# Performance work log

Hardware: AMD Instinct MI355X
Metric: run time of the kernel (lower is better)

Reference implementation:

```python
import jax, jax.numpy as jnp
import numpy as np

B, S, HID = 2, 2048, 2048
H, KV, D = 16, 4, 128
EPS = 1e-6


def rms_norm(x, w, eps=EPS):
    # Qwen3.5 convention: (1 + weight) * RMSNorm(x), weight init 0
    v = jnp.mean(x * x, axis=-1, keepdims=True)
    return (1.0 + w) * (x * jax.lax.rsqrt(v + eps))


def rotate_half(x):
    x1, x2 = jnp.split(x, 2, axis=-1)
    return jnp.concatenate([-x2, x1], axis=-1)


def apply_rope(x, cos, sin):
    # x: [B,S,h,D]; cos/sin: [S,D]
    c = cos[None, :, None, :]
    s = sin[None, :, None, :]
    return x * c + rotate_half(x) * s


def setup_inputs():
    key = jax.random.key(0)
    ks = jax.random.split(key, 8)
    sc = 0.02
    hidden_states = jax.random.normal(ks[0], (B, S, HID), jnp.float32)
    past_key_value = jnp.zeros((B, 2, KV, S, D), jnp.float32)
    pos = jnp.arange(S, dtype=jnp.float32)
    inv_freq = 1.0 / (10000.0 ** (jnp.arange(0, D, 2, dtype=jnp.float32) / D))
    ang = pos[:, None] * inv_freq[None, :]                    # [S, D/2]
    cos = jnp.concatenate([jnp.cos(ang), jnp.cos(ang)], -1)   # [S, D]
    sin = jnp.concatenate([jnp.sin(ang), jnp.sin(ang)], -1)
    rope_rotary_cos_sin = jnp.stack([cos, sin], axis=1)       # [S, 2, D]
    context_lengths = jnp.full((B,), S, dtype=jnp.int32)
    kvcache_start_index = jnp.zeros((B,), dtype=jnp.int32)
    Wq = jax.random.normal(ks[1], (HID, H * D * 2), jnp.float32) * sc
    Wk = jax.random.normal(ks[2], (HID, KV * D), jnp.float32) * sc
    Wv = jax.random.normal(ks[3], (HID, KV * D), jnp.float32) * sc
    Wo = jax.random.normal(ks[4], (H * D, HID), jnp.float32) * sc
    q_norm_w = jax.random.normal(ks[5], (D,), jnp.float32) * sc
    k_norm_w = jax.random.normal(ks[6], (D,), jnp.float32) * sc
    return {"hidden_states": hidden_states, "past_key_value": past_key_value,
            "rope_rotary_cos_sin": rope_rotary_cos_sin,
            "context_lengths": context_lengths,
            "kvcache_start_index": kvcache_start_index,
            "Wq": Wq, "Wk": Wk, "Wv": Wv, "Wo": Wo,
            "q_norm_w": q_norm_w, "k_norm_w": k_norm_w}


def reference(hidden_states, past_key_value, rope_rotary_cos_sin,
              context_lengths, kvcache_start_index,
              Wq, Wk, Wv, Wo, q_norm_w, k_norm_w):
    # projections
    q_out = jnp.einsum('bsc,cd->bsd', hidden_states, Wq).reshape(B, S, H, 2 * D)
    query, gate = jnp.split(q_out, 2, axis=-1)                # each [B,S,H,D]
    k = jnp.einsum('bsc,cd->bsd', hidden_states, Wk).reshape(B, S, KV, D)
    v = jnp.einsum('bsc,cd->bsd', hidden_states, Wv).reshape(B, S, KV, D)
    # per-head QK RMSNorm
    query = rms_norm(query, q_norm_w)
    k = rms_norm(k, k_norm_w)
    # RoPE
    cos, sin = rope_rotary_cos_sin[:, 0, :], rope_rotary_cos_sin[:, 1, :]
    query = apply_rope(query, cos, sin)
    k = apply_rope(k, cos, sin)
    # write KV cache (prefill at start index 0)
    present = past_key_value.at[:, 0, :, :S, :].set(jnp.transpose(k, (0, 2, 1, 3)))
    present = present.at[:, 1, :, :S, :].set(jnp.transpose(v, (0, 2, 1, 3)))
    # GQA causal attention
    group = H // KV
    k_r = jnp.repeat(k, group, axis=2)                        # [B,S,H,D]
    v_r = jnp.repeat(v, group, axis=2)
    scores = jnp.einsum('bqhd,bkhd->bhqk', query, k_r) / jnp.sqrt(jnp.float32(D))
    causal = jnp.tril(jnp.ones((S, S), dtype=bool))
    scores = jnp.where(causal[None, None], scores, jnp.float32(-1e30))
    probs = jax.nn.softmax(scores, axis=-1)
    attn = jnp.einsum('bhqk,bkhd->bqhd', probs, v_r)          # [B,S,H,D]
    # sigmoid gating + output proj
    attn = attn * jax.nn.sigmoid(gate)
    out = jnp.einsum('bsd,dc->bsc', attn.reshape(B, S, H * D), Wo)
    return out, present
```

## Files before the change

### kernel.cpp

```cpp
#include <hip/hip_runtime.h>
#include <hip/hip_bf16.h>
#include <cstdint>
#include <cstddef>

#define BB   2
#define SS   2048
#define HIDD 2048
#define HH   16
#define KVH  4
#define DD   128
#define NQKV 5120
#define MM   4096

typedef unsigned short u16t;
typedef __attribute__((ext_vector_type(8))) short s16x8;
typedef __attribute__((ext_vector_type(4))) short s16x4;
typedef __attribute__((ext_vector_type(4))) float f32x4;

__device__ __forceinline__ u16t f2bf(float f) {
  unsigned u = __float_as_uint(f);
  u += 0x7fffu + ((u >> 16) & 1u);
  return (u16t)(u >> 16);
}
__device__ __forceinline__ float bf2f(u16t h) {
  return __uint_as_float(((unsigned)h) << 16);
}
__device__ __forceinline__ void gload_lds16(const void* g, void* l) {
  __builtin_amdgcn_global_load_lds(
      (const __attribute__((address_space(1))) unsigned int*)g,
      (__attribute__((address_space(3))) unsigned int*)l, 16, 0, 0);
}
__device__ __forceinline__ unsigned cvtpk_bf16(float lo, float hi) {
  unsigned r;
  asm("v_cvt_pk_bf16_f32 %0, %1, %2" : "=v"(r) : "v"(lo), "v"(hi));
  return r;
}
__device__ __forceinline__ f32x4 fmax4(f32x4 a, f32x4 b) {
  f32x4 r;
  r[0] = fmaxf(a[0], b[0]); r[1] = fmaxf(a[1], b[1]);
  r[2] = fmaxf(a[2], b[2]); r[3] = fmaxf(a[3], b[3]);
  return r;
}
template <int N>
__device__ __forceinline__ void waitvm() {
  static_assert(N == 0 || N == 3 || N == 4 || N == 6 || N == 8, "add literal");
  if constexpr (N == 0)      asm volatile("s_waitcnt vmcnt(0)" ::: "memory");
  else if constexpr (N == 3) asm volatile("s_waitcnt vmcnt(3)" ::: "memory");
  else if constexpr (N == 4) asm volatile("s_waitcnt vmcnt(4)" ::: "memory");
  else if constexpr (N == 6) asm volatile("s_waitcnt vmcnt(6)" ::: "memory");
  else if constexpr (N == 8) asm volatile("s_waitcnt vmcnt(8)" ::: "memory");
}

__global__ __launch_bounds__(256) void prep_all(const float* __restrict__ hidden,
                                                const float* __restrict__ Wq,
                                                const float* __restrict__ Wk,
                                                const float* __restrict__ Wv,
                                                const float* __restrict__ Wo,
                                                u16t* __restrict__ Xb,
                                                u16t* __restrict__ Wt,
                                                u16t* __restrict__ Wot) {
  __shared__ float lds[64 * 65];
  int bid = blockIdx.x;
  int t = threadIdx.x;
  if (bid < 4096) {
    size_t i = ((size_t)bid * 256 + t) * 8;
    f32x4 v0 = *(const f32x4*)(hidden + i);
    f32x4 v1 = *(const f32x4*)(hidden + i + 4);
    s16x8 o;
    o[0] = (short)f2bf(v0[0]); o[1] = (short)f2bf(v0[1]);
    o[2] = (short)f2bf(v0[2]); o[3] = (short)f2bf(v0[3]);
    o[4] = (short)f2bf(v1[0]); o[5] = (short)f2bf(v1[1]);
    o[6] = (short)f2bf(v1[2]); o[7] = (short)f2bf(v1[3]);
    *(s16x8*)(Xb + i) = o;
    return;
  }
  bid -= 4096;
  const float* src; u16t* dst; int N;
  if (bid < 2048)      { src = Wq; dst = Wt;                         N = 4096; }
  else if (bid < 2304) { src = Wk; dst = Wt + (size_t)4096 * HIDD;   N = 512;  bid -= 2048; }
  else if (bid < 2560) { src = Wv; dst = Wt + (size_t)4608 * HIDD;   N = 512;  bid -= 2304; }
  else                 { src = Wo; dst = Wot;                        N = 2048; bid -= 2560; }
  const int ktiles = HIDD / 64;
  int n0 = (bid / ktiles) << 6;
  int k0 = (bid % ktiles) << 6;
#pragma unroll
  for (int i = 0; i < 16; i++) {
    int idx = i * 256 + t;
    int r = idx >> 6, c = idx & 63;
    lds[c * 65 + r] = src[(size_t)(k0 + r) * N + n0 + c];
  }
  __syncthreads();
#pragma unroll
  for (int i = 0; i < 2; i++) {
    int idx = i * 256 + t;
    int rr = idx >> 3, k8 = (idx & 7) * 8;
    s16x8 o;
#pragma unroll
    for (int e = 0; e < 8; e++) o[e] = (short)f2bf(lds[rr * 65 + k8 + e]);
    *(s16x8*)(dst + (size_t)(n0 + rr) * HIDD + k0 + k8) = o;
  }
}

__device__ __forceinline__ s16x8 ldsfrag(const char* half, int r, int g) {
  return *(const s16x8*)(half + r * 64 + ((g ^ ((r >> 1) & 3)) << 4));
}
template <int NL>
__device__ __forceinline__ void stage_half(char* ldsbase, const u16t* gbase,
                                           int K, int kcol, int tid) {
#pragma unroll
  for (int i = 0; i < NL; i++) {
    int o16 = i * 512 + tid;
    int r = o16 >> 2;
    int cs = (o16 & 3) ^ ((r >> 1) & 3);
    gload_lds16(gbase + (size_t)r * K + kcol + cs * 8, ldsbase + o16 * 16);
  }
}

template <int BN, typename CT>
__global__ __launch_bounds__(512, 2) void gemm8(const u16t* __restrict__ A,
                                                const u16t* __restrict__ Bt,
                                                CT* __restrict__ C,
                                                int M, int N, int K) {
  constexpr int NLB = BN / 128;
  constexpr int AHALF = 16384, ASLOT = 32768;
  constexpr int BHALF = BN * 64, BSLOT = 2 * BHALF;
  constexpr int PAIR = 2 + NLB;
  constexpr int NI = BN / 64;
  extern __shared__ __align__(16) char lds[];
  char* As = lds;
  char* Bs = lds + 2 * ASLOT;
  int tid = threadIdx.x, lane = tid & 63, w = tid >> 6;
  int wm = w >> 2, wn = w & 3;
  int cpx = gridDim.x >> 3;
  int wgid = (blockIdx.x & 7) * cpx + (blockIdx.x >> 3);
  int bm = wgid & 15, bn = wgid >> 4;
  int m0 = bm << 8, n0 = bn * BN;
  const u16t* Ag = A + (size_t)m0 * K;
  const u16t* Bg = Bt + (size_t)n0 * K;
  const int NT = K >> 6;

  stage_half<2>(As, Ag, K, 0, tid);
  stage_half<NLB>(Bs, Bg, K, 0, tid);
  stage_half<2>(As + AHALF, Ag, K, 32, tid);
  stage_half<NLB>(Bs + BHALF, Bg, K, 32, tid);
  stage_half<2>(As + ASLOT, Ag, K, 64, tid);
  stage_half<NLB>(Bs + BSLOT, Bg, K, 64, tid);
  waitvm<2 * PAIR>();
  __builtin_amdgcn_s_barrier();

  const f32x4 fz = {0.f, 0.f, 0.f, 0.f};
  f32x4 acc[8][NI];
#pragma unroll
  for (int i = 0; i < 8; i++)
#pragma unroll
    for (int j = 0; j < NI; j++) acc[i][j] = fz;
  s16x8 afr[4], bfr[NI];
  int g = lane >> 4;
  int rA = (lane & 15) + wm * 128;
  int rB = (lane & 15) + wn * (BN / 4);

  for (int kt = 0; kt < NT; kt++) {
    int cur = kt & 1;
    char* Acur = As + cur * ASLOT;
    char* Bcur = Bs + cur * BSLOT;
    char* Anxt = As + (cur ^ 1) * ASLOT;
    char* Bnxt = Bs + (cur ^ 1) * BSLOT;
#pragma unroll
    for (int ni = 0; ni < NI; ni++) bfr[ni] = ldsfrag(Bcur, rB + ni * 16, g);
#pragma unroll
    for (int mi = 0; mi < 4; mi++) afr[mi] = ldsfrag(Acur, rA + mi * 16, g);
    if (kt + 1 < NT) stage_half<2>(Anxt + AHALF, Ag, K, (kt + 1) * 64 + 32, tid);
    __builtin_amdgcn_s_barrier();
    asm volatile("s_waitcnt lgkmcnt(0)" ::: "memory");
    __builtin_amdgcn_s_setprio(1);
#pragma unroll
    for (int mi = 0; mi < 4; mi++)
#pragma unroll
      for (int ni = 0; ni < NI; ni++)
        acc[mi][ni] = __builtin_amdgcn_mfma_f32_16x16x32_bf16(afr[mi], bfr[ni], acc[mi][ni], 0, 0, 0);
    __builtin_amdgcn_s_setprio(0);
    __builtin_amdgcn_s_barrier();
#pragma unroll
    for (int mi = 0; mi < 4; mi++) afr[mi] = ldsfrag(Acur, rA + 64 + mi * 16, g);
    if (kt + 1 < NT) stage_half<NLB>(Bnxt + BHALF, Bg, K, (kt + 1) * 64 + 32, tid);
    __builtin_amdgcn_s_barrier();
    asm volatile("s_waitcnt lgkmcnt(0)" ::: "memory");
    __builtin_amdgcn_s_setprio(1);
#pragma unroll
    for (int mi = 0; mi < 4; mi++)
#pragma unroll
      for (int ni = 0; ni < NI; ni++)
        acc[4 + mi][ni] = __builtin_amdgcn_mfma_f32_16x16x32_bf16(afr[mi], bfr[ni], acc[4 + mi][ni], 0, 0, 0);
    __builtin_amdgcn_s_setprio(0);
    if (kt + 1 < NT) waitvm<2 * PAIR>();
    else             waitvm<0>();
    __builtin_amdgcn_s_barrier();
#pragma unroll
    for (int ni = 0; ni < NI; ni++) bfr[ni] = ldsfrag(Bcur + BHALF, rB + ni * 16, g);
#pragma unroll
    for (int mi = 0; mi < 4; mi++) afr[mi] = ldsfrag(Acur + AHALF, rA + mi * 16, g);
    if (kt + 2 < NT) stage_half<2>(Acur, Ag, K, (kt + 2) * 64, tid);
    __builtin_amdgcn_s_barrier();
    asm volatile("s_waitcnt lgkmcnt(0)" ::: "memory");
    __builtin_amdgcn_s_setprio(1);
#pragma unroll
    for (int mi = 0; mi < 4; mi++)
#pragma unroll
      for (int ni = 0; ni < NI; ni++)
        acc[mi][ni] = __builtin_amdgcn_mfma_f32_16x16x32_bf16(afr[mi], bfr[ni], acc[mi][ni], 0, 0, 0);
    __builtin_amdgcn_s_setprio(0);
    __builtin_amdgcn_s_barrier();
#pragma unroll
    for (int mi = 0; mi < 4; mi++) afr[mi] = ldsfrag(Acur + AHALF, rA + 64 + mi * 16, g);
    if (kt + 2 < NT) stage_half<NLB>(Bcur, Bg, K, (kt + 2) * 64, tid);
    __builtin_amdgcn_s_barrier();
    asm volatile("s_waitcnt lgkmcnt(0)" ::: "memory");
    __builtin_amdgcn_s_setprio(1);
#pragma unroll
    for (int mi = 0; mi < 4; mi++)
#pragma unroll
      for (int ni = 0; ni < NI; ni++)
        acc[4 + mi][ni] = __builtin_amdgcn_mfma_f32_16x16x32_bf16(afr[mi], bfr[ni], acc[4 + mi][ni], 0, 0, 0);
    __builtin_amdgcn_s_setprio(0);
    if (kt < NT - 1) {
      if (kt + 2 < NT) waitvm<2 * PAIR>();
      else             waitvm<PAIR>();
    }
    __builtin_amdgcn_s_barrier();
  }
#pragma unroll
  for (int mi = 0; mi < 8; mi++)
#pragma unroll
    for (int ni = 0; ni < NI; ni++) {
      int row0 = m0 + wm * 128 + mi * 16 + ((lane >> 4) << 2);
      int col = n0 + wn * (BN / 4) + ni * 16 + (lane & 15);
#pragma unroll
      for (int j = 0; j < 4; j++) {
        if constexpr (sizeof(CT) == 2)
          C[(size_t)(row0 + j) * N + col] = f2bf(acc[mi][ni][j]);
        else
          C[(size_t)(row0 + j) * N + col] = acc[mi][ni][j];
      }
    }
}

__global__ __launch_bounds__(256) void gemm_kv(const u16t* __restrict__ A,
                                               const u16t* __restrict__ Bt,
                                               u16t* __restrict__ Cqkv,
                                               float* __restrict__ present,
                                               u16t* __restrict__ Vtb,
                                               int K) {
  __shared__ __align__(16) char As[128 * 64];
  __shared__ __align__(16) char Bs[128 * 64];
  int tid = threadIdx.x;
  int lane = tid & 63;
  int w = tid >> 6;
  int cpx = gridDim.x >> 3;
  int wgid = ((int)blockIdx.x & 7) * cpx + ((int)blockIdx.x >> 3);
  const int mtiles = MM >> 7;
  int bm = wgid % mtiles;
  int bn = wgid / mtiles;
  int m0 = bm << 7, n0 = bn << 7;
  int wr = (w >> 1) * 64, wc = (w & 1) * 64;

  const f32x4 fz = {0.f, 0.f, 0.f, 0.f};
  f32x4 acc[4][4];
#pragma unroll
  for (int i = 0; i < 4; i++)
#pragma unroll
    for (int j = 0; j < 4; j++) acc[i][j] = fz;

  for (int k0 = 0; k0 < K; k0 += 32) {
    __syncthreads();
#pragma unroll
    for (int i = 0; i < 2; i++) {
      int idx = i * 256 + tid;
      int r = idx >> 2, c = idx & 3;
      int csrc = c ^ ((r >> 1) & 3);
      gload_lds16(A + (size_t)(m0 + r) * K + k0 + csrc * 8, As + idx * 16);
      gload_lds16(Bt + (size_t)(n0 + r) * K + k0 + csrc * 8, Bs + idx * 16);
    }
    __syncthreads();
    s16x8 af[4], bf[4];
    int g = lane >> 4;
#pragma unroll
    for (int mi = 0; mi < 4; mi++) {
      int r = wr + mi * 16 + (lane & 15);
      af[mi] = *(const s16x8*)(As + r * 64 + ((g ^ ((r >> 1) & 3)) << 4));
    }
#pragma unroll
    for (int ni = 0; ni < 4; ni++) {
      int r = wc + ni * 16 + (lane & 15);
      bf[ni] = *(const s16x8*)(Bs + r * 64 + ((g ^ ((r >> 1) & 3)) << 4));
    }
#pragma unroll
    for (int mi = 0; mi < 4; mi++)
#pragma unroll
      for (int ni = 0; ni < 4; ni++)
        acc[mi][ni] = __builtin_amdgcn_mfma_f32_16x16x32_bf16(af[mi], bf[ni], acc[mi][ni], 0, 0, 0);
  }
  if (bn < 4) {
#pragma unroll
    for (int mi = 0; mi < 4; mi++)
#pragma unroll
      for (int ni = 0; ni < 4; ni++) {
        int row0 = m0 + wr + mi * 16 + ((lane >> 4) << 2);
        int col = n0 + wc + ni * 16 + (lane & 15);
#pragma unroll
        for (int j = 0; j < 4; j++)
          Cqkv[(size_t)(row0 + j) * NQKV + 4096 + col] = f2bf(acc[mi][ni][j]);
      }
  } else {
#pragma unroll
    for (int mi = 0; mi < 4; mi++)
#pragma unroll
      for (int ni = 0; ni < 4; ni++) {
        int row0 = m0 + wr + mi * 16 + ((lane >> 4) << 2);
        int vcol = (n0 - 512) + wc + ni * 16 + (lane & 15);
        int kv = vcol >> 7, d = vcol & 127;
        int bb = row0 >> 11, sp = row0 & 2047;
        size_t pbase = (((size_t)(bb * 2 * KVH + KVH + kv)) * SS + sp) * DD + d;
#pragma unroll
        for (int j = 0; j < 4; j++)
          present[pbase + (size_t)j * DD] = acc[mi][ni][j];
        s16x4 pk;
        pk[0] = (short)f2bf(acc[mi][ni][0]);
        pk[1] = (short)f2bf(acc[mi][ni][1]);
        pk[2] = (short)f2bf(acc[mi][ni][2]);
        pk[3] = (short)f2bf(acc[mi][ni][3]);
        *(s16x4*)(Vtb + ((size_t)(bb * KVH + kv) * DD + d) * SS + sp) = pk;
      }
  }
}

__global__ __launch_bounds__(256) void qk_norm_rope(const u16t* __restrict__ Cqkv,
                                                    const float* __restrict__ rope,
                                                    const float* __restrict__ qw,
                                                    const float* __restrict__ kw,
                                                    u16t* __restrict__ Qb,
                                                    u16t* __restrict__ Kb,
                                                    u16t* __restrict__ Gs,
                                                    float* __restrict__ present) {
  int wid = blockIdx.x * 4 + (threadIdx.x >> 6);
  int lane = threadIdx.x & 63;
  const int NQ = BB * SS * HH;
  if (wid < NQ) {
    int b = wid >> 15;
    int rem = wid & 32767;
    int s = rem >> 4, h = rem & 15;
    const u16t* base = Cqkv + (size_t)(b * SS + s) * NQKV + h * 256;
    float xlo = bf2f(base[lane]), xhi = bf2f(base[64 + lane]);
    float ss = xlo * xlo + xhi * xhi;
    ss += __shfl_xor(ss, 1);  ss += __shfl_xor(ss, 2);  ss += __shfl_xor(ss, 4);
    ss += __shfl_xor(ss, 8);  ss += __shfl_xor(ss, 16); ss += __shfl_xor(ss, 32);
    float r = rsqrtf(ss * (1.f / 128.f) + 1e-6f);
    float qlo = xlo * r * (1.f + qw[lane]);
    float qhi = xhi * r * (1.f + qw[64 + lane]);
    const float* cs = rope + (size_t)s * 256;
    float clo = cs[lane], chi = cs[64 + lane];
    float slo = cs[128 + lane], shi = cs[192 + lane];
    const float SC = 0.08838834764831845f * 1.4426950408889634f;
    float olo = (qlo * clo - qhi * slo) * SC;
    float ohi = (qhi * chi + qlo * shi) * SC;
    size_t qoff = (((size_t)b * HH + h) * SS + s) * DD;
    Qb[qoff + lane] = f2bf(olo);
    Qb[qoff + 64 + lane] = f2bf(ohi);
    float glo = bf2f(base[128 + lane]), ghi = bf2f(base[192 + lane]);
    size_t goff = ((size_t)(b * SS + s)) * (HH * DD) + h * DD;
    Gs[goff + lane] = f2bf(1.f / (1.f + __expf(-glo)));
    Gs[goff + 64 + lane] = f2bf(1.f / (1.f + __expf(-ghi)));
  } else {
    int wid2 = wid - NQ;
    int b = wid2 >> 13;
    int rem = wid2 & 8191;
    int s = rem >> 2, kv = rem & 3;
    const u16t* base = Cqkv + (size_t)(b * SS + s) * NQKV + 4096 + kv * 128;
    float xlo = bf2f(base[lane]), xhi = bf2f(base[64 + lane]);
    float ss = xlo * xlo + xhi * xhi;
    ss += __shfl_xor(ss, 1);  ss += __shfl_xor(ss, 2);  ss += __shfl_xor(ss, 4);
    ss += __shfl_xor(ss, 8);  ss += __shfl_xor(ss, 16); ss += __shfl_xor(ss, 32);
    float r = rsqrtf(ss * (1.f / 128.f) + 1e-6f);
    float klo = xlo * r * (1.f + kw[lane]);
    float khi = xhi * r * (1.f + kw[64 + lane]);
    const float* cs = rope + (size_t)s * 256;
    float clo = cs[lane], chi = cs[64 + lane];
    float slo = cs[128 + lane], shi = cs[192 + lane];
    float olo = klo * clo - khi * slo;
    float ohi = khi * chi + klo * shi;
    size_t koff = (((size_t)b * KVH + kv) * SS + s) * DD;
    Kb[koff + lane] = f2bf(olo);
    Kb[koff + 64 + lane] = f2bf(ohi);
    size_t poff = (((size_t)(b * 2 * KVH + kv)) * SS + s) * DD;
    present[poff + lane] = olo;
    present[poff + 64 + lane] = ohi;
  }
}

__global__ __launch_bounds__(256, 2) void attn_kernel(const u16t* __restrict__ Qb,
                                                      const u16t* __restrict__ Kb,
                                                      const u16t* __restrict__ Vtb,
                                                      const u16t* __restrict__ Gs,
                                                      u16t* __restrict__ AttG) {
  __shared__ __align__(16) char Ks[2 * 16384];
  __shared__ __align__(16) char Vs[2 * 16384];
  __shared__ __align__(16) char Ps[4 * 2048];

  int tid = threadIdx.x, lane = tid & 63, w = tid >> 6;
  int x = blockIdx.x & 7;
  int b = x >> 2, kv = x & 3;
  int rr = blockIdx.x >> 3;
  int h = kv * 4 + (rr & 3);
  int p = rr >> 2;

  const u16t* Kbase = Kb + (((size_t)(b * KVH + kv)) * SS) * DD;
  const u16t* Vbase = Vtb + (((size_t)(b * KVH + kv)) * DD) * SS;

  auto stageK = [&](int kt, int buf) {
#pragma unroll
    for (int i = 0; i < 4; i++) {
      int idx = i * 256 + tid;
      int r_ = idx >> 4, c_ = idx & 15;
      gload_lds16(Kbase + (size_t)(kt * 64 + r_) * DD + (c_ ^ (r_ & 7)) * 8,
                  Ks + buf * 16384 + idx * 16);
    }
  };
  auto stageV = [&](int kt, int buf) {
#pragma unroll
    for (int i = 0; i < 4; i++) {
      int idx = i * 256 + tid;
      int r_ = idx >> 3, c_ = idx & 7;
      gload_lds16(Vbase + (size_t)r_ * SS + kt * 64 + (c_ ^ (r_ & 7)) * 8,
                  Vs + buf * 16384 + idx * 16);
    }
  };

  const f32x4 fz = {0.f, 0.f, 0.f, 0.f};
  int g = lane >> 4;
  int q15 = lane & 15;
  int q7 = q15 & 7;
  char* pq = Ps + w * 2048 + q15 * 128;
  int cur = 0;

  int ka[4][4];
#pragma unroll
  for (int ni = 0; ni < 4; ni++)
#pragma unroll
    for (int ks = 0; ks < 4; ks++)
      ka[ni][ks] = (ni * 16 + q15) * 256 + (((ks * 4 + g) ^ q7) << 4);
  int va[2][8];
#pragma unroll
  for (int ks2 = 0; ks2 < 2; ks2++)
#pragma unroll
    for (int f = 0; f < 8; f++)
      va[ks2][f] = (f * 16 + q15) * 128 + (((ks2 * 4 + g) ^ q7) << 4);
  int pr_[2];
#pragma unroll
  for (int ks2 = 0; ks2 < 2; ks2++) pr_[ks2] = ((ks2 * 4 + g) ^ q7) << 4;
  int pw_[4];
#pragma unroll
  for (int ni = 0; ni < 4; ni++)
    pw_[ni] = (((ni * 2 + (g >> 1)) ^ q7) << 4) + ((g & 1) << 3);

  stageK(0, 0);
  stageV(0, 0);

  for (int seg = 0; seg < 2; seg++) {
    int qt = (seg == 0) ? (31 - p) : p;
    const u16t* Qbase = Qb + (((size_t)(b * HH + h)) * SS + qt * 64) * DD;
    s16x8 qf[4];
    {
      const u16t* qrow = Qbase + (size_t)(w * 16 + q15) * DD + g * 8;
#pragma unroll
      for (int ks = 0; ks < 4; ks++) qf[ks] = *(const s16x8*)(qrow + ks * 32);
    }
    f32x4 acco[8];
#pragma unroll
    for (int f = 0; f < 8; f++) acco[f] = fz;
    float mrun = -INFINITY, lrun = 0.f;

    if (seg == 0) {
      asm volatile("s_waitcnt vmcnt(0)" ::: "memory");
      __builtin_amdgcn_s_barrier();
    }

    for (int kt = 0; kt <= qt; kt++) {
      bool havenext = (kt < qt) || (seg == 0);
      if (havenext) {
        int nk = (kt < qt) ? (kt + 1) : 0;
        stageK(nk, cur ^ 1);
        stageV(nk, cur ^ 1);
      }
      const char* kc = Ks + (cur << 14);
      const char* vc = Vs + (cur << 14);
      f32x4 accs[4];
#pragma unroll
      for (int ni = 0; ni < 4; ni++) accs[ni] = fz;
#pragma unroll
      for (int ni = 0; ni < 4; ni++)
#pragma unroll
        for (int ks = 0; ks < 4; ks++) {
          s16x8 bfk = *(const s16x8*)(kc + ka[ni][ks]);
          accs[ni] = __builtin_amdgcn_mfma_f32_16x16x32_bf16(bfk, qf[ks], accs[ni], 0, 0, 0);
        }
      if (kt == qt) {
        int ql = w * 16 + q15;
#pragma unroll
        for (int ni = 0; ni < 4; ni++)
#pragma unroll
          for (int j = 0; j < 4; j++) {
            int kl = ni * 16 + (g << 2) + j;
            if (kl > ql) accs[ni][j] = -1e30f;
          }
      }
      f32x4 m4 = fmax4(fmax4(accs[0], accs[1]), fmax4(accs[2], accs[3]));
      float mt = fmaxf(fmaxf(m4[0], m4[1]), fmaxf(m4[2], m4[3]));
      mt = fmaxf(mt, __shfl_xor(mt, 16));
      mt = fmaxf(mt, __shfl_xor(mt, 32));
      float mnew = fmaxf(mrun, mt);
      float alpha = __builtin_amdgcn_exp2f(mrun - mnew);
      mrun = mnew;
#pragma unroll
      for (int ni = 0; ni < 4; ni++)
#pragma unroll
        for (int j = 0; j < 4; j++)
          accs[ni][j] = __builtin_amdgcn_exp2f(accs[ni][j] - mnew);
      f32x4 s4 = (accs[0] + accs[1]) + (accs[2] + accs[3]);
      float rs = (s4[0] + s4[1]) + (s4[2] + s4[3]);
      rs += __shfl_xor(rs, 16);
      rs += __shfl_xor(rs, 32);
      lrun = lrun * alpha + rs;
      float ar[4];
#pragma unroll
      for (int j = 0; j < 4; j++) ar[j] = __shfl(alpha, (g << 2) + j);
#pragma unroll
      for (int f = 0; f < 8; f++)
#pragma unroll
        for (int j = 0; j < 4; j++) acco[f][j] *= ar[j];

#pragma unroll
      for (int ni = 0; ni < 4; ni++) {
        uint2 pk;
        pk.x = cvtpk_bf16(accs[ni][0], accs[ni][1]);
        pk.y = cvtpk_bf16(accs[ni][2], accs[ni][3]);
        *(uint2*)(pq + pw_[ni]) = pk;
      }
#pragma unroll
      for (int ks2 = 0; ks2 < 2; ks2++) {
        s16x8 pa = *(const s16x8*)(pq + pr_[ks2]);
#pragma unroll
        for (int f = 0; f < 8; f++) {
          s16x8 vf = *(const s16x8*)(vc + va[ks2][f]);
          acco[f] = __builtin_amdgcn_mfma_f32_16x16x32_bf16(pa, vf, acco[f], 0, 0, 0);
        }
      }
      if (havenext) {
        asm volatile("s_waitcnt vmcnt(0)" ::: "memory");
        __builtin_amdgcn_s_barrier();
        cur ^= 1;
      }
    }
    float lr[4];
#pragma unroll
    for (int j = 0; j < 4; j++) lr[j] = __shfl(lrun, (g << 2) + j);
#pragma unroll
    for (int f = 0; f < 8; f++) {
      int d = f * 16 + q15;
#pragma unroll
      for (int j = 0; j < 4; j++) {
        int srow = qt * 64 + w * 16 + (g << 2) + j;
        float o = acco[f][j] / lr[j];
        size_t off = ((size_t)b * SS + srow) * (HH * DD) + h * DD + d;
        float gt = bf2f(Gs[off]);
        AttG[off] = f2bf(o * gt);
      }
    }
  }
}

extern "C" void kernel_launch(void* const* d_in, const int* in_sizes, int n_in,
                              void* d_out, int out_size, void* d_ws, size_t ws_size,
                              hipStream_t stream) {
  const float* hidden = (const float*)d_in[0];
  const float* rope   = (const float*)d_in[2];
  const float* Wq     = (const float*)d_in[5];
  const float* Wk     = (const float*)d_in[6];
  const float* Wv     = (const float*)d_in[7];
  const float* Wo     = (const float*)d_in[8];
  const float* qw     = (const float*)d_in[9];
  const float* kw     = (const float*)d_in[10];
  float* out = (float*)d_out;
  float* present = out + (size_t)BB * SS * HIDD;

  char* ws = (char*)d_ws;
  u16t* Xb    = (u16t*)(ws);
  u16t* Wt    = (u16t*)(ws + 16777216);
  u16t* Wot   = (u16t*)(ws + 37748736);
  u16t* Cqkv  = (u16t*)(ws + 46137344);
  u16t* Qb    = (u16t*)(ws + 88080384);
  u16t* Kb    = (u16t*)(ws + 104857600);
  u16t* Vtb   = (u16t*)(ws + 109051904);
  u16t* Gs    = (u16t*)(ws + 113246208);
  u16t* AttG  = Xb;

  (void)hipFuncSetAttribute(reinterpret_cast<const void*>(gemm8<256, u16t>),
                            hipFuncAttributeMaxDynamicSharedMemorySize, 131072);
  (void)hipFuncSetAttribute(reinterpret_cast<const void*>(gemm8<128, float>),
                            hipFuncAttributeMaxDynamicSharedMemorySize, 98304);

  prep_all<<<4096 + 3584, 256, 0, stream>>>(hidden, Wq, Wk, Wv, Wo, Xb, Wt, Wot);
  gemm8<256, u16t><<<(MM / 256) * (4096 / 256), 512, 131072, stream>>>(Xb, Wt, Cqkv, MM, NQKV, HIDD);
  gemm_kv<<<(MM / 128) * (1024 / 128), 256, 0, stream>>>(
      Xb, Wt + (size_t)4096 * HIDD, Cqkv, present, Vtb, HIDD);
  qk_norm_rope<<<(BB * SS * (HH + KVH)) / 4, 256, 0, stream>>>(Cqkv, rope, qw, kw, Qb, Kb, Gs, present);
  attn_kernel<<<BB * HH * (SS / 128), 256, 0, stream>>>(Qb, Kb, Vtb, Gs, AttG);
  gemm8<128, float><<<(MM / 256) * (HIDD / 128), 512, 98304, stream>>>(AttG, Wot, out, MM, HIDD, HIDD);
}
```

Baseline: 265.5 us.

## Fuse Q RMSNorm, RoPE and gate sigmoid into the Q projection GEMM epilogue

Adds a gemm8q kernel in which each 256-column tile covers one head's 128 query columns plus its 128 gate columns. The query half is staged through swizzled LDS so each row can be RMS-normalized, rotated with RoPE and written straight to Qb. The gate half gets its sigmoid applied and goes straight to Gs. This removes the bf16 round trip of Q and the gate through Cqkv and shrinks the separate norm kernel to K heads only. In exchange the GEMM epilogue gets longer, runs per-row serial loops and does extra LDS traffic.

```diff
diff --git a/kernel.cpp b/kernel.cpp
--- a/kernel.cpp
+++ b/kernel.cpp
@@ -244,6 +244,179 @@
     }
 }
 
+__global__ __launch_bounds__(512, 2) void gemm8q(const u16t* __restrict__ A,
+                                                 const u16t* __restrict__ Bt,
+                                                 const float* __restrict__ rope,
+                                                 const float* __restrict__ qw,
+                                                 u16t* __restrict__ Qb,
+                                                 u16t* __restrict__ Gs,
+                                                 int K) {
+  constexpr int NLB = 2, AHALF = 16384, ASLOT = 32768;
+  constexpr int BHALF = 16384, BSLOT = 32768;
+  constexpr int PAIR = 4, NI = 4;
+  extern __shared__ __align__(16) char lds[];
+  char* As = lds;
+  char* Bs = lds + 2 * ASLOT;
+  int tid = threadIdx.x, lane = tid & 63, w = tid >> 6;
+  int wm = w >> 2, wn = w & 3;
+  int cpx = gridDim.x >> 3;
+  int wgid = (blockIdx.x & 7) * cpx + (blockIdx.x >> 3);
+  int bm = wgid & 15, bn = wgid >> 4;
+  int m0 = bm << 8, n0 = bn << 8;
+  const u16t* Ag = A + (size_t)m0 * K;
+  const u16t* Bg = Bt + (size_t)n0 * K;
+  const int NT = K >> 6;
+
+  stage_half<2>(As, Ag, K, 0, tid);
+  stage_half<NLB>(Bs, Bg, K, 0, tid);
+  stage_half<2>(As + AHALF, Ag, K, 32, tid);
+  stage_half<NLB>(Bs + BHALF, Bg, K, 32, tid);
+  stage_half<2>(As + ASLOT, Ag, K, 64, tid);
+  stage_half<NLB>(Bs + BSLOT, Bg, K, 64, tid);
+  waitvm<2 * PAIR>();
+  __builtin_amdgcn_s_barrier();
+
+  const f32x4 fz = {0.f, 0.f, 0.f, 0.f};
+  f32x4 acc[8][NI];
+#pragma unroll
+  for (int i = 0; i < 8; i++)
+#pragma unroll
+    for (int j = 0; j < NI; j++) acc[i][j] = fz;
+  s16x8 afr[4], bfr[NI];
+  int g = lane >> 4;
+  int rA = (lane & 15) + wm * 128;
+  int rB = (lane & 15) + wn * 64;
+
+  for (int kt = 0; kt < NT; kt++) {
+    int cur = kt & 1;
+    char* Acur = As + cur * ASLOT;
+    char* Bcur = Bs + cur * BSLOT;
+    char* Anxt = As + (cur ^ 1) * ASLOT;
+    char* Bnxt = Bs + (cur ^ 1) * BSLOT;
+#pragma unroll
+    for (int ni = 0; ni < NI; ni++) bfr[ni] = ldsfrag(Bcur, rB + ni * 16, g);
+#pragma unroll
+    for (int mi = 0; mi < 4; mi++) afr[mi] = ldsfrag(Acur, rA + mi * 16, g);
+    if (kt + 1 < NT) stage_half<2>(Anxt + AHALF, Ag, K, (kt + 1) * 64 + 32, tid);
+    __builtin_amdgcn_s_barrier();
+    asm volatile("s_waitcnt lgkmcnt(0)" ::: "memory");
+    __builtin_amdgcn_s_setprio(1);
+#pragma unroll
+    for (int mi = 0; mi < 4; mi++)
+#pragma unroll
+      for (int ni = 0; ni < NI; ni++)
+        acc[mi][ni] = __builtin_amdgcn_mfma_f32_16x16x32_bf16(afr[mi], bfr[ni], acc[mi][ni], 0, 0, 0);
+    __builtin_amdgcn_s_setprio(0);
+    __builtin_amdgcn_s_barrier();
+#pragma unroll
+    for (int mi = 0; mi < 4; mi++) afr[mi] = ldsfrag(Acur, rA + 64 + mi * 16, g);
+    if (kt + 1 < NT) stage_half<NLB>(Bnxt + BHALF, Bg, K, (kt + 1) * 64 + 32, tid);
+    __builtin_amdgcn_s_barrier();
+    asm volatile("s_waitcnt lgkmcnt(0)" ::: "memory");
+    __builtin_amdgcn_s_setprio(1);
+#pragma unroll
+    for (int mi = 0; mi < 4; mi++)
+#pragma unroll
+      for (int ni = 0; ni < NI; ni++)
+        acc[4 + mi][ni] = __builtin_amdgcn_mfma_f32_16x16x32_bf16(afr[mi], bfr[ni], acc[4 + mi][ni], 0, 0, 0);
+    __builtin_amdgcn_s_setprio(0);
+    if (kt + 1 < NT) waitvm<2 * PAIR>();
+    else             waitvm<0>();
+    __builtin_amdgcn_s_barrier();
+#pragma unroll
+    for (int ni = 0; ni < NI; ni++) bfr[ni] = ldsfrag(Bcur + BHALF, rB + ni * 16, g);
+#pragma unroll
+    for (int mi = 0; mi < 4; mi++) afr[mi] = ldsfrag(Acur + AHALF, rA + mi * 16, g);
+    if (kt + 2 < NT) stage_half<2>(Acur, Ag, K, (kt + 2) * 64, tid);
+    __builtin_amdgcn_s_barrier();
+    asm volatile("s_waitcnt lgkmcnt(0)" ::: "memory");
+    __builtin_amdgcn_s_setprio(1);
+#pragma unroll
+    for (int mi = 0; mi < 4; mi++)
+#pragma unroll
+      for (int ni = 0; ni < NI; ni++)
+        acc[mi][ni] = __builtin_amdgcn_mfma_f32_16x16x32_bf16(afr[mi], bfr[ni], acc[mi][ni], 0, 0, 0);
+    __builtin_amdgcn_s_setprio(0);
+    __builtin_amdgcn_s_barrier();
+#pragma unroll
+    for (int mi = 0; mi < 4; mi++) afr[mi] = ldsfrag(Acur + AHALF, rA + 64 + mi * 16, g);
+    if (kt + 2 < NT) stage_half<NLB>(Bcur, Bg, K, (kt + 2) * 64, tid);
+    __builtin_amdgcn_s_barrier();
+    asm volatile("s_waitcnt lgkmcnt(0)" ::: "memory");
+    __builtin_amdgcn_s_setprio(1);
+#pragma unroll
+    for (int mi = 0; mi < 4; mi++)
+#pragma unroll
+      for (int ni = 0; ni < NI; ni++)
+        acc[4 + mi][ni] = __builtin_amdgcn_mfma_f32_16x16x32_bf16(afr[mi], bfr[ni], acc[4 + mi][ni], 0, 0, 0);
+    __builtin_amdgcn_s_setprio(0);
+    if (kt < NT - 1) {
+      if (kt + 2 < NT) waitvm<2 * PAIR>();
+      else             waitvm<PAIR>();
+    }
+    __builtin_amdgcn_s_barrier();
+  }
+
+  int h = bn;
+  float* qbuf = (float*)lds;
+  if (wn < 2) {
+#pragma unroll
+    for (int mi = 0; mi < 8; mi++)
+#pragma unroll
+      for (int ni = 0; ni < NI; ni++) {
+        int rl0 = wm * 128 + mi * 16 + ((lane >> 4) << 2);
+        int c = wn * 64 + ni * 16 + (lane & 15);
+        int gr = c >> 4;
+#pragma unroll
+        for (int j = 0; j < 4; j++) {
+          int rl = rl0 + j;
+          qbuf[rl * 128 + (((gr ^ ((rl >> 2) & 7)) << 4) | (c & 15))] = acc[mi][ni][j];
+        }
+      }
+  } else {
+#pragma unroll
+    for (int mi = 0; mi < 8; mi++)
+#pragma unroll
+      for (int ni = 0; ni < NI; ni++) {
+        int row0 = m0 + wm * 128 + mi * 16 + ((lane >> 4) << 2);
+        int d = (wn - 2) * 64 + ni * 16 + (lane & 15);
+#pragma unroll
+        for (int j = 0; j < 4; j++) {
+          int bb = (row0 + j) >> 11, s = (row0 + j) & 2047;
+          float gv = acc[mi][ni][j];
+          Gs[((size_t)(bb * SS + s)) * (HH * DD) + h * DD + d] =
+              f2bf(1.f / (1.f + __expf(-gv)));
+        }
+      }
+  }
+  __syncthreads();
+  float qwl = qw[lane], qwh = qw[64 + lane];
+  const float SC = 0.08838834764831845f * 1.4426950408889634f;
+  for (int r2 = 0; r2 < 32; r2++) {
+    int rl = w * 32 + r2;
+    int row0 = m0 + rl;
+    int bb = row0 >> 11, s = row0 & 2047;
+    int swz = ((rl >> 2) & 7) << 4;
+    int cl = lane, ch = 64 + lane;
+    float xlo = qbuf[rl * 128 + ((((cl >> 4) << 4) ^ swz) | (cl & 15))];
+    float xhi = qbuf[rl * 128 + ((((ch >> 4) << 4) ^ swz) | (ch & 15))];
+    float ss2 = xlo * xlo + xhi * xhi;
+    ss2 += __shfl_xor(ss2, 1);  ss2 += __shfl_xor(ss2, 2);  ss2 += __shfl_xor(ss2, 4);
+    ss2 += __shfl_xor(ss2, 8);  ss2 += __shfl_xor(ss2, 16); ss2 += __shfl_xor(ss2, 32);
+    float r = rsqrtf(ss2 * (1.f / 128.f) + 1e-6f);
+    float qlo = xlo * r * (1.f + qwl);
+    float qhi = xhi * r * (1.f + qwh);
+    const float* cs = rope + (size_t)s * 256;
+    float clo = cs[lane], chi = cs[64 + lane];
+    float slo = cs[128 + lane], shi = cs[192 + lane];
+    float olo = (qlo * clo - qhi * slo) * SC;
+    float ohi = (qhi * chi + qlo * shi) * SC;
+    size_t qoff = (((size_t)bb * HH + h) * SS + s) * DD;
+    Qb[qoff + lane] = f2bf(olo);
+    Qb[qoff + 64 + lane] = f2bf(ohi);
+  }
+}
+
 __global__ __launch_bounds__(256) void gemm_kv(const u16t* __restrict__ A,
                                                const u16t* __restrict__ Bt,
                                                u16t* __restrict__ Cqkv,
@@ -333,67 +506,35 @@
   }
 }
 
-__global__ __launch_bounds__(256) void qk_norm_rope(const u16t* __restrict__ Cqkv,
-                                                    const float* __restrict__ rope,
-                                                    const float* __restrict__ qw,
-                                                    const float* __restrict__ kw,
-                                                    u16t* __restrict__ Qb,
-                                                    u16t* __restrict__ Kb,
-                                                    u16t* __restrict__ Gs,
-                                                    float* __restrict__ present) {
+__global__ __launch_bounds__(256) void k_norm_rope(const u16t* __restrict__ Cqkv,
+                                                   const float* __restrict__ rope,
+                                                   const float* __restrict__ kw,
+                                                   u16t* __restrict__ Kb,
+                                                   float* __restrict__ present) {
   int wid = blockIdx.x * 4 + (threadIdx.x >> 6);
   int lane = threadIdx.x & 63;
-  const int NQ = BB * SS * HH;
-  if (wid < NQ) {
-    int b = wid >> 15;
-    int rem = wid & 32767;
-    int s = rem >> 4, h = rem & 15;
-    const u16t* base = Cqkv + (size_t)(b * SS + s) * NQKV + h * 256;
-    float xlo = bf2f(base[lane]), xhi = bf2f(base[64 + lane]);
-    float ss = xlo * xlo + xhi * xhi;
-    ss += __shfl_xor(ss, 1);  ss += __shfl_xor(ss, 2);  ss += __shfl_xor(ss, 4);
-    ss += __shfl_xor(ss, 8);  ss += __shfl_xor(ss, 16); ss += __shfl_xor(ss, 32);
-    float r = rsqrtf(ss * (1.f / 128.f) + 1e-6f);
-    float qlo = xlo * r * (1.f + qw[lane]);
-    float qhi = xhi * r * (1.f + qw[64 + lane]);
-    const float* cs = rope + (size_t)s * 256;
-    float clo = cs[lane], chi = cs[64 + lane];
-    float slo = cs[128 + lane], shi = cs[192 + lane];
-    const float SC = 0.08838834764831845f * 1.4426950408889634f;
-    float olo = (qlo * clo - qhi * slo) * SC;
-    float ohi = (qhi * chi + qlo * shi) * SC;
-    size_t qoff = (((size_t)b * HH + h) * SS + s) * DD;
-    Qb[qoff + lane] = f2bf(olo);
-    Qb[qoff + 64 + lane] = f2bf(ohi);
-    float glo = bf2f(base[128 + lane]), ghi = bf2f(base[192 + lane]);
-    size_t goff = ((size_t)(b * SS + s)) * (HH * DD) + h * DD;
-    Gs[goff + lane] = f2bf(1.f / (1.f + __expf(-glo)));
-    Gs[goff + 64 + lane] = f2bf(1.f / (1.f + __expf(-ghi)));
-  } else {
-    int wid2 = wid - NQ;
-    int b = wid2 >> 13;
-    int rem = wid2 & 8191;
-    int s = rem >> 2, kv = rem & 3;
-    const u16t* base = Cqkv + (size_t)(b * SS + s) * NQKV + 4096 + kv * 128;
-    float xlo = bf2f(base[lane]), xhi = bf2f(base[64 + lane]);
-    float ss = xlo * xlo + xhi * xhi;
-    ss += __shfl_xor(ss, 1);  ss += __shfl_xor(ss, 2);  ss += __shfl_xor(ss, 4);
-    ss += __shfl_xor(ss, 8);  ss += __shfl_xor(ss, 16); ss += __shfl_xor(ss, 32);
-    float r = rsqrtf(ss * (1.f / 128.f) + 1e-6f);
-    float klo = xlo * r * (1.f + kw[lane]);
-    float khi = xhi * r * (1.f + kw[64 + lane]);
-    const float* cs = rope + (size_t)s * 256;
-    float clo = cs[lane], chi = cs[64 + lane];
-    float slo = cs[128 + lane], shi = cs[192 + lane];
-    float olo = klo * clo - khi * slo;
-    float ohi = khi * chi + klo * shi;
-    size_t koff = (((size_t)b * KVH + kv) * SS + s) * DD;
-    Kb[koff + lane] = f2bf(olo);
-    Kb[koff + 64 + lane] = f2bf(ohi);
-    size_t poff = (((size_t)(b * 2 * KVH + kv)) * SS + s) * DD;
-    present[poff + lane] = olo;
-    present[poff + 64 + lane] = ohi;
-  }
+  int b = wid >> 13;
+  int rem = wid & 8191;
+  int s = rem >> 2, kv = rem & 3;
+  const u16t* base = Cqkv + (size_t)(b * SS + s) * NQKV + 4096 + kv * 128;
+  float xlo = bf2f(base[lane]), xhi = bf2f(base[64 + lane]);
+  float ss = xlo * xlo + xhi * xhi;
+  ss += __shfl_xor(ss, 1);  ss += __shfl_xor(ss, 2);  ss += __shfl_xor(ss, 4);
+  ss += __shfl_xor(ss, 8);  ss += __shfl_xor(ss, 16); ss += __shfl_xor(ss, 32);
+  float r = rsqrtf(ss * (1.f / 128.f) + 1e-6f);
+  float klo = xlo * r * (1.f + kw[lane]);
+  float khi = xhi * r * (1.f + kw[64 + lane]);
+  const float* cs = rope + (size_t)s * 256;
+  float clo = cs[lane], chi = cs[64 + lane];
+  float slo = cs[128 + lane], shi = cs[192 + lane];
+  float olo = klo * clo - khi * slo;
+  float ohi = khi * chi + klo * shi;
+  size_t koff = (((size_t)b * KVH + kv) * SS + s) * DD;
+  Kb[koff + lane] = f2bf(olo);
+  Kb[koff + 64 + lane] = f2bf(ohi);
+  size_t poff = (((size_t)(b * 2 * KVH + kv)) * SS + s) * DD;
+  present[poff + lane] = olo;
+  present[poff + 64 + lane] = ohi;
 }
 
 __global__ __launch_bounds__(256, 2) void attn_kernel(const u16t* __restrict__ Qb,
@@ -602,16 +743,16 @@
   u16t* Gs    = (u16t*)(ws + 113246208);
   u16t* AttG  = Xb;
 
-  (void)hipFuncSetAttribute(reinterpret_cast<const void*>(gemm8<256, u16t>),
+  (void)hipFuncSetAttribute(reinterpret_cast<const void*>(gemm8q),
                             hipFuncAttributeMaxDynamicSharedMemorySize, 131072);
   (void)hipFuncSetAttribute(reinterpret_cast<const void*>(gemm8<128, float>),
                             hipFuncAttributeMaxDynamicSharedMemorySize, 98304);
 
   prep_all<<<4096 + 3584, 256, 0, stream>>>(hidden, Wq, Wk, Wv, Wo, Xb, Wt, Wot);
-  gemm8<256, u16t><<<(MM / 256) * (4096 / 256), 512, 131072, stream>>>(Xb, Wt, Cqkv, MM, NQKV, HIDD);
+  gemm8q<<<(MM / 256) * (4096 / 256), 512, 131072, stream>>>(Xb, Wt, rope, qw, Qb, Gs, HIDD);
   gemm_kv<<<(MM / 128) * (1024 / 128), 256, 0, stream>>>(
       Xb, Wt + (size_t)4096 * HIDD, Cqkv, present, Vtb, HIDD);
-  qk_norm_rope<<<(BB * SS * (HH + KVH)) / 4, 256, 0, stream>>>(Cqkv, rope, qw, kw, Qb, Kb, Gs, present);
+  k_norm_rope<<<(BB * SS * KVH) / 4, 256, 0, stream>>>(Cqkv, rope, kw, Kb, present);
   attn_kernel<<<BB * HH * (SS / 128), 256, 0, stream>>>(Qb, Kb, Vtb, Gs, AttG);
   gemm8<128, float><<<(MM / 256) * (HIDD / 128), 512, 98304, stream>>>(AttG, Wot, out, MM, HIDD, HIDD);
 }
```

New measurement: 262.6 us. No clear change (-1.1%).
